# Kernel optimization log

Measured on AMD Instinct MI355X. Metric: run time of the kernel, lower is better.

## Reference

```python
import jax, jax.numpy as jnp
import numpy as np

B, S, H, NH = 2, 2048, 1024, 16
HD = H // NH
R = 4
LORA_SCALE = 16.0 / 4.0  # lora_alpha / r


def lora_linear(x, W, b, A, Bm):
    # x: [b,t,in]; W: [out,in]; A: [r,in]; Bm: [out,r]
    base = jnp.einsum('bti,oi->bto', x, W) + b
    lora = jnp.einsum('btr,or->bto', jnp.einsum('bti,ri->btr', x, A), Bm)
    return base + LORA_SCALE * lora


def setup_inputs() -> dict:
    key = jax.random.key(0)
    ks = jax.random.split(key, 14)
    std = 1.0 / np.sqrt(H)
    d = {
        'hidden_states': jax.random.normal(ks[0], (B, S, H), dtype=jnp.float32),
        'attention_mask': jnp.zeros((B, 1, 1, S), dtype=jnp.float32),
    }
    for i, nm in enumerate(['q', 'k', 'v']):
        d[f'W{nm}'] = jax.random.normal(ks[1 + 4 * i], (H, H), dtype=jnp.float32) * std
        d[f'b{nm}'] = jnp.zeros((H,), dtype=jnp.float32)
        d[f'A{nm}'] = jax.random.normal(ks[2 + 4 * i], (R, H), dtype=jnp.float32) * std
        d[f'B{nm}'] = jnp.zeros((H, R), dtype=jnp.float32) + 0.01 * jax.random.normal(ks[3 + 4 * i], (H, R), dtype=jnp.float32)
    return d


def reference(hidden_states, attention_mask, Wq, bq, Aq, Bq, Wk, bk, Ak, Bk, Wv, bv, Av, Bv):
    def heads(p):  # [b,t,(h d)] -> [b,h,t,d]
        return p.reshape(B, S, NH, HD).transpose(0, 2, 1, 3)

    q = heads(lora_linear(hidden_states, Wq, bq, Aq, Bq))
    k = heads(lora_linear(hidden_states, Wk, bk, Ak, Bk))
    v = heads(lora_linear(hidden_states, Wv, bv, Av, Bv))

    scores = jnp.einsum('bhqd,bhkd->bhqk', q, k) / jnp.sqrt(jnp.float32(HD))
    causal = jnp.tril(jnp.ones((S, S), dtype=scores.dtype))
    causal = (1.0 - causal) * -10000.0  # [S,S], broadcast over b,h
    scores = scores + attention_mask + causal[None, None]
    weights = jax.nn.softmax(scores, axis=-1)  # dropout p=0 -> identity (eval)
    ctx = jnp.einsum('bhqk,bhkd->bhqd', weights, v)
    return ctx.transpose(0, 2, 1, 3).reshape(B, S, H)
```

## Files before the change

kernel.cpp:

```cpp
#include <hip/hip_runtime.h>
#include <stdint.h>

#define B_ 2
#define S_ 2048
#define H_ 1024
#define NH_ 16
#define HD_ 64
#define M_ 4096
#define LOG2E 1.44269504089f

typedef unsigned short u16;
typedef __bf16 bf16x8 __attribute__((ext_vector_type(8)));
typedef float  f32x4  __attribute__((ext_vector_type(4)));

#if __has_builtin(__builtin_amdgcn_exp2f)
#define EXP2(x) __builtin_amdgcn_exp2f(x)
#else
#define EXP2(x) exp2f(x)
#endif

#define WAITV4() asm volatile("s_waitcnt vmcnt(4)" ::: "memory")
#define WAITV0() asm volatile("s_waitcnt vmcnt(0)" ::: "memory")
#define SCHED0() __builtin_amdgcn_sched_barrier(0)

__device__ inline u16 f2bf(float f) {
  union { float f; uint32_t u; } a; a.f = f;
  uint32_t r = a.u + 0x7FFFu + ((a.u >> 16) & 1u);
  return (u16)(r >> 16);
}

__device__ inline void gload_lds16(const void* g, void* l) {
  __builtin_amdgcn_global_load_lds((const __attribute__((address_space(1))) void*)g,
                                   (__attribute__((address_space(3))) void*)l, 16, 0, 0);
}

__global__ __launch_bounds__(256) void cvt_kernel(
    const float* __restrict__ x,
    const float* __restrict__ wq, const float* __restrict__ wk, const float* __restrict__ wv,
    const float* __restrict__ Aq, const float* __restrict__ Ak, const float* __restrict__ Av,
    const float* __restrict__ LBq, const float* __restrict__ LBk, const float* __restrict__ LBv,
    const float* __restrict__ amask,
    u16* __restrict__ xbf, u16* __restrict__ wbf, float* __restrict__ maskl2e) {
  const int XN = M_ * H_;
  const int WN = H_ * H_;
  const int total = XN + 3 * WN;
  int idx = (blockIdx.x * 256 + threadIdx.x) * 4;
  if (idx < XN) {
    float4 v = *(const float4*)(x + idx);
    *(ushort4*)(xbf + idx) = make_ushort4(f2bf(v.x), f2bf(v.y), f2bf(v.z), f2bf(v.w));
  } else if (idx < total) {
    int j = idx - XN; int p = j >> 20; int off = j & (WN - 1);
    const float* W  = (p == 0) ? wq : (p == 1 ? wk : wv);
    const float* A  = (p == 0) ? Aq : (p == 1 ? Ak : Av);
    const float* LB = (p == 0) ? LBq : (p == 1 ? LBk : LBv);
    int n = off >> 10, k = off & 1023;
    float4 v  = *(const float4*)(W + off);
    f32x4 lb  = *(const f32x4*)&LB[n * 4];
    float4 a0 = *(const float4*)(A + k);
    float4 a1 = *(const float4*)(A + 1024 + k);
    float4 a2 = *(const float4*)(A + 2048 + k);
    float4 a3 = *(const float4*)(A + 3072 + k);
    v.x += 4.f * (lb.x * a0.x + lb.y * a1.x + lb.z * a2.x + lb.w * a3.x);
    v.y += 4.f * (lb.x * a0.y + lb.y * a1.y + lb.z * a2.y + lb.w * a3.y);
    v.z += 4.f * (lb.x * a0.z + lb.y * a1.z + lb.z * a2.z + lb.w * a3.z);
    v.w += 4.f * (lb.x * a0.w + lb.y * a1.w + lb.z * a2.w + lb.w * a3.w);
    *(ushort4*)(wbf + (p << 20) + off) = make_ushort4(f2bf(v.x), f2bf(v.y), f2bf(v.z), f2bf(v.w));
  } else {
    int mi = idx - total;
    if (mi < B_ * S_) {
      float4 mv = *(const float4*)(amask + mi);
      mv.x *= LOG2E; mv.y *= LOG2E; mv.z *= LOG2E; mv.w *= LOG2E;
      *(float4*)(maskl2e + mi) = mv;
    }
  }
}

template<int P>
__device__ __forceinline__ void gemm_body(
    const u16* __restrict__ xbf, const u16* __restrict__ wbf,
    const float* __restrict__ bias, u16* __restrict__ qkv,
    u16* __restrict__ As, u16* __restrict__ Bs) {
  const int n0 = blockIdx.x * 128;
  const int m0 = blockIdx.y * 128;
  const u16* Wp = wbf + (P << 20);
  const int tid = threadIdx.x, lane = tid & 63, w = tid >> 6;
  const int g = lane >> 4, q15 = lane & 15;
  const int wr = w >> 1, wc = w & 1;
  const f32x4 fzero = {0.f, 0.f, 0.f, 0.f};
  f32x4 acc[4][4];
#pragma unroll
  for (int mi = 0; mi < 4; ++mi)
#pragma unroll
    for (int ni = 0; ni < 4; ++ni) acc[mi][ni] = fzero;
  const int srow = lane >> 2;

  auto STAGE = [&](int buf, int k0) {
#pragma unroll
    for (int j = 0; j < 2; ++j) {
      int c = w * 2 + j;
      int row = c * 16 + srow;
      int uu = (lane & 3) ^ ((row >> 1) & 3);
      gload_lds16(xbf + (size_t)(m0 + row) * 1024 + k0 + uu * 8, As + buf * 4096 + c * 512);
      gload_lds16(Wp  + (size_t)(n0 + row) * 1024 + k0 + uu * 8, Bs + buf * 4096 + c * 512);
    }
  };

  STAGE(0, 0);
  STAGE(1, 32);
  int c0 = 0, c1 = 1, c2 = 2;
#pragma unroll 1
  for (int t = 0; t < 32; ++t) {
    if (t < 31) WAITV4(); else WAITV0();
    SCHED0();
    __builtin_amdgcn_s_barrier();
    if (t + 2 < 32) STAGE(c2, (t + 2) * 32);
    const u16* Ab = As + c0 * 4096;
    const u16* Bb = Bs + c0 * 4096;
    bf16x8 af[4], bfr[4];
#pragma unroll
    for (int mi = 0; mi < 4; ++mi) {
      int r = wr * 64 + mi * 16 + q15;
      af[mi] = *(const bf16x8*)&Ab[r * 32 + ((g ^ ((r >> 1) & 3)) * 8)];
    }
#pragma unroll
    for (int ni = 0; ni < 4; ++ni) {
      int r = wc * 64 + ni * 16 + q15;
      bfr[ni] = *(const bf16x8*)&Bb[r * 32 + ((g ^ ((r >> 1) & 3)) * 8)];
    }
    __builtin_amdgcn_s_setprio(1);
#pragma unroll
    for (int mi = 0; mi < 4; ++mi)
#pragma unroll
      for (int ni = 0; ni < 4; ++ni) {
        if (P == 2)
          acc[mi][ni] = __builtin_amdgcn_mfma_f32_16x16x32_bf16(af[mi], bfr[ni], acc[mi][ni], 0, 0, 0);
        else
          acc[mi][ni] = __builtin_amdgcn_mfma_f32_16x16x32_bf16(bfr[ni], af[mi], acc[mi][ni], 0, 0, 0);
      }
    __builtin_amdgcn_s_setprio(0);
    int tmp = c0; c0 = c1; c1 = c2; c2 = tmp;
  }

  if (P != 2) {
#pragma unroll
    for (int ni = 0; ni < 4; ++ni) {
      int nb = n0 + wc * 64 + ni * 16 + g * 4;
      f32x4 bi = *(const f32x4*)&bias[nb];
      int h = nb >> 6, dbase = nb & 63;
#pragma unroll
      for (int mi = 0; mi < 4; ++mi) {
        int m = m0 + wr * 64 + mi * 16 + q15;
        int bb = m >> 11, s = m & 2047;
        size_t bhs = (size_t)(bb * 16 + h) * 2048 + s;
        float v0 = acc[mi][ni][0] + bi.x, v1 = acc[mi][ni][1] + bi.y;
        float v2 = acc[mi][ni][2] + bi.z, v3 = acc[mi][ni][3] + bi.w;
        size_t addr;
        if (P == 0) {
          const float qs = 0.125f * LOG2E;
          v0 *= qs; v1 *= qs; v2 *= qs; v3 *= qs;
          addr = bhs * 64 + dbase;
        } else {
          int pos = (((dbase >> 3) ^ (s & 7)) << 3) | (dbase & 7);
          addr = 4194304 + bhs * 64 + pos;
        }
        *(ushort4*)&qkv[addr] = make_ushort4(f2bf(v0), f2bf(v1), f2bf(v2), f2bf(v3));
      }
    }
  } else {
    float biasv[4];
#pragma unroll
    for (int ni = 0; ni < 4; ++ni) biasv[ni] = bias[n0 + wc * 64 + ni * 16 + q15];
#pragma unroll
    for (int mi = 0; mi < 4; ++mi) {
      int mbase = m0 + wr * 64 + mi * 16 + g * 4;
      int bb = mbase >> 11, sbase = mbase & 2047;
      int sr = sbase & 31;
      int cba = (((sr >> 4) & 1) << 2) | (((sr >> 2) & 3) << 3);
      int sp = (sbase & 32) | cba;
#pragma unroll
      for (int ni = 0; ni < 4; ++ni) {
        int n = n0 + wc * 64 + ni * 16 + q15;
        int d = n & 63, h = n >> 6;
        int spp = (((sp >> 3) ^ (d & 7)) << 3) | (sp & 7);
        size_t addr = 8388608 + ((size_t)(bb * 16 + h) * 64 + d) * 2048 + (sbase & ~63) + spp;
        *(ushort4*)&qkv[addr] = make_ushort4(
            f2bf(acc[mi][ni][0] + biasv[ni]), f2bf(acc[mi][ni][1] + biasv[ni]),
            f2bf(acc[mi][ni][2] + biasv[ni]), f2bf(acc[mi][ni][3] + biasv[ni]));
      }
    }
  }
}

__global__ __launch_bounds__(256) void qkv_gemm(
    const u16* __restrict__ xbf, const u16* __restrict__ wbf,
    const float* __restrict__ bq, const float* __restrict__ bk, const float* __restrict__ bv,
    u16* __restrict__ qkv) {
  __shared__ __align__(16) u16 As[3 * 4096];
  __shared__ __align__(16) u16 Bs[3 * 4096];
  switch (blockIdx.z) {
    case 0: gemm_body<0>(xbf, wbf, bq, qkv, As, Bs); break;
    case 1: gemm_body<1>(xbf, wbf, bk, qkv, As, Bs); break;
    default: gemm_body<2>(xbf, wbf, bv, qkv, As, Bs); break;
  }
}

__global__ __launch_bounds__(256, 2) void attn_kernel(
    const u16* __restrict__ qkv, const float* __restrict__ maskl2e, float* __restrict__ out) {
  const int bid = blockIdx.x;
  const int bh = (bid & 7) * 4 + ((bid >> 3) & 3);
  const int qt = 15 - (bid >> 5);
  const int b = bh >> 4, h = bh & 15;
  const int tid = threadIdx.x, lane = tid & 63, w = tid >> 6;
  const int g = lane >> 4, ql = lane & 15;
  const u16* Qb = qkv + (size_t)bh * 131072;
  const u16* Kb = qkv + 4194304 + (size_t)bh * 131072;
  const u16* Vb = qkv + 8388608 + (size_t)bh * 131072;
  const float* Mb = maskl2e + b * 2048;
  __shared__ __align__(16) u16 Ks[2][64][64];
  __shared__ __align__(16) u16 Vs[2][64][64];

  auto STAGE = [&](int nb, int kb) {
#pragma unroll
    for (int j = 0; j < 2; ++j) {
      int rl = w * 16 + j * 8 + (lane >> 3);
      gload_lds16(Kb + (size_t)(kb + rl) * 64 + (lane & 7) * 8, &Ks[nb][w * 16 + j * 8][0]);
      gload_lds16(Vb + (size_t)rl * 2048 + kb + (lane & 7) * 8, &Vs[nb][w * 16 + j * 8][0]);
    }
  };

  const int qbase = qt * 128 + w * 32;
  bf16x8 qf[2][2];
#pragma unroll
  for (int qg = 0; qg < 2; ++qg)
#pragma unroll
    for (int ks = 0; ks < 2; ++ks)
      qf[qg][ks] = *(const bf16x8*)&Qb[(size_t)(qbase + qg * 16 + ql) * 64 + ks * 32 + g * 8];
  const f32x4 fzero = {0.f, 0.f, 0.f, 0.f};
  f32x4 acc[2][4];
#pragma unroll
  for (int qg = 0; qg < 2; ++qg)
#pragma unroll
    for (int dt = 0; dt < 4; ++dt) acc[qg][dt] = fzero;
  float mrun[2] = {-1e30f, -1e30f}, lrun[2] = {0.f, 0.f};
  const int nt = 2 * qt + 2;

  f32x4 mkC[4], mkN[4];
  STAGE(0, 0);
#pragma unroll
  for (int k16 = 0; k16 < 4; ++k16) mkC[k16] = *(const f32x4*)&Mb[k16 * 16 + g * 4];

#pragma unroll 1
  for (int t = 0; t < nt; ++t) {
    WAITV0();
    SCHED0();
    __builtin_amdgcn_s_barrier();
    const int kb = t * 64;
    if (t + 1 < nt) {
      STAGE((t + 1) & 1, kb + 64);
#pragma unroll
      for (int k16 = 0; k16 < 4; ++k16) mkN[k16] = *(const f32x4*)&Mb[kb + 64 + k16 * 16 + g * 4];
    }
    const int cb = t & 1;
    f32x4 st[2][4];
    __builtin_amdgcn_s_setprio(1);
#pragma unroll
    for (int k16 = 0; k16 < 4; ++k16) {
      bf16x8 kf0 = *(const bf16x8*)&Ks[cb][k16 * 16 + ql][(g ^ (ql & 7)) * 8];
      bf16x8 kf1 = *(const bf16x8*)&Ks[cb][k16 * 16 + ql][((4 + g) ^ (ql & 7)) * 8];
      st[0][k16] = __builtin_amdgcn_mfma_f32_16x16x32_bf16(kf0, qf[0][0], mkC[k16], 0, 0, 0);
      st[0][k16] = __builtin_amdgcn_mfma_f32_16x16x32_bf16(kf1, qf[0][1], st[0][k16], 0, 0, 0);
      st[1][k16] = __builtin_amdgcn_mfma_f32_16x16x32_bf16(kf0, qf[1][0], mkC[k16], 0, 0, 0);
      st[1][k16] = __builtin_amdgcn_mfma_f32_16x16x32_bf16(kf1, qf[1][1], st[1][k16], 0, 0, 0);
    }
    __builtin_amdgcn_s_setprio(0);
    bf16x8 pfv[2][2];
#pragma unroll
    for (int qg = 0; qg < 2; ++qg) {
      const int qq = qbase + qg * 16 + ql;
      const bool needm = (kb + 63 > qbase + qg * 16);
      float sc[16];
#pragma unroll
      for (int k16 = 0; k16 < 4; ++k16)
#pragma unroll
        for (int r = 0; r < 4; ++r) {
          float sv = st[qg][k16][r];
          if (needm) { int key = kb + k16 * 16 + g * 4 + r; sv = (key > qq) ? -1e30f : sv; }
          sc[k16 * 4 + r] = sv;
        }
      float m8[8], m4[4];
#pragma unroll
      for (int i = 0; i < 8; ++i) m8[i] = fmaxf(sc[i], sc[i + 8]);
#pragma unroll
      for (int i = 0; i < 4; ++i) m4[i] = fmaxf(m8[i], m8[i + 4]);
      float pmax = fmaxf(fmaxf(m4[0], m4[1]), fmaxf(m4[2], m4[3]));
      if (!__all(pmax <= mrun[qg] + 8.f)) {
        float pm = fmaxf(pmax, __shfl_xor(pmax, 16, 64));
        pm = fmaxf(pm, __shfl_xor(pm, 32, 64));
        const float mt = fmaxf(mrun[qg], pm);
        const float scale = EXP2(mrun[qg] - mt);
        lrun[qg] *= scale;
#pragma unroll
        for (int dt = 0; dt < 4; ++dt) acc[qg][dt] *= scale;
        mrun[qg] = mt;
      }
      float pv[16];
#pragma unroll
      for (int i = 0; i < 16; ++i) pv[i] = EXP2(sc[i] - mrun[qg]);
      float s8[8], s4[4];
#pragma unroll
      for (int i = 0; i < 8; ++i) s8[i] = pv[i] + pv[i + 8];
#pragma unroll
      for (int i = 0; i < 4; ++i) s4[i] = s8[i] + s8[i + 4];
      lrun[qg] += (s4[0] + s4[1]) + (s4[2] + s4[3]);
#pragma unroll
      for (int ksub = 0; ksub < 2; ++ksub)
#pragma unroll
        for (int j = 0; j < 4; ++j) {
          pfv[qg][ksub][j]     = (__bf16)pv[ksub * 8 + j];
          pfv[qg][ksub][4 + j] = (__bf16)pv[ksub * 8 + 4 + j];
        }
    }
    __builtin_amdgcn_s_setprio(1);
#pragma unroll
    for (int dt = 0; dt < 4; ++dt)
#pragma unroll
      for (int ksub = 0; ksub < 2; ++ksub) {
        bf16x8 vf = *(const bf16x8*)&Vs[cb][dt * 16 + ql][((ksub * 4 + g) ^ (ql & 7)) * 8];
        acc[0][dt] = __builtin_amdgcn_mfma_f32_16x16x32_bf16(vf, pfv[0][ksub], acc[0][dt], 0, 0, 0);
        acc[1][dt] = __builtin_amdgcn_mfma_f32_16x16x32_bf16(vf, pfv[1][ksub], acc[1][dt], 0, 0, 0);
      }
    __builtin_amdgcn_s_setprio(0);
#pragma unroll
    for (int k16 = 0; k16 < 4; ++k16) mkC[k16] = mkN[k16];
  }

#pragma unroll
  for (int qg = 0; qg < 2; ++qg) {
    float lsum = lrun[qg];
    lsum += __shfl_xor(lsum, 16, 64);
    lsum += __shfl_xor(lsum, 32, 64);
    const float inv = 1.f / lsum;
    const int qq = qbase + qg * 16 + ql;
#pragma unroll
    for (int dt = 0; dt < 4; ++dt) {
      f32x4 o = acc[qg][dt] * inv;
      *(f32x4*)&out[((size_t)b * 2048 + qq) * 1024 + h * 64 + dt * 16 + g * 4] = o;
    }
  }
}

extern "C" void kernel_launch(void* const* d_in, const int* in_sizes, int n_in,
                              void* d_out, int out_size, void* d_ws, size_t ws_size,
                              hipStream_t stream) {
  const float* x  = (const float*)d_in[0];
  const float* am = (const float*)d_in[1];
  const float* Wq = (const float*)d_in[2];
  const float* bq = (const float*)d_in[3];
  const float* Aq = (const float*)d_in[4];
  const float* Bq = (const float*)d_in[5];
  const float* Wk = (const float*)d_in[6];
  const float* bk = (const float*)d_in[7];
  const float* Ak = (const float*)d_in[8];
  const float* Bk = (const float*)d_in[9];
  const float* Wv = (const float*)d_in[10];
  const float* bv = (const float*)d_in[11];
  const float* Av = (const float*)d_in[12];
  const float* Bv = (const float*)d_in[13];
  float* out = (float*)d_out;

  u16* xbf   = (u16*)d_ws;
  u16* wbf   = xbf + 4194304;
  u16* qkv   = wbf + 3145728;
  float* mk  = (float*)(qkv + 12582912);

  cvt_kernel<<<7172, 256, 0, stream>>>(x, Wq, Wk, Wv, Aq, Ak, Av, Bq, Bk, Bv, am, xbf, wbf, mk);
  qkv_gemm<<<dim3(8, 32, 3), 256, 0, stream>>>(xbf, wbf, bq, bk, bv, qkv);
  attn_kernel<<<512, 256, 0, stream>>>(qkv, mk, out);
}
```

Before: 106.1 us.

## Split causal attention into balanced per-wave key chunks with a merge pass

Each wave now handles a pair of 32-row query groups (p and 63-p) and a fixed slice of 11 key tiles, which balances the causal work across waves. Partial accumulators are stored as bf16 in reused workspace and the m/l statistics in a side buffer, and a new merge kernel combines them with log-sum-exp weights. K/V are loaded straight from global memory into registers instead of being staged through LDS with barriers, and occupancy rises to three blocks per CU. The cost is an extra kernel launch, extra global traffic for the partials, and lower precision in the bf16 partial accumulators.

```diff
diff --git a/kernel.cpp b/kernel.cpp
--- a/kernel.cpp
+++ b/kernel.cpp
@@ -27,6 +27,9 @@
   union { float f; uint32_t u; } a; a.f = f;
   uint32_t r = a.u + 0x7FFFu + ((a.u >> 16) & 1u);
   return (u16)(r >> 16);
+}
+__device__ inline float bf2f(u16 v) {
+  union { uint32_t u; float f; } a; a.u = ((uint32_t)v) << 16; return a.f;
 }
 
 __device__ inline void gload_lds16(const void* g, void* l) {
@@ -204,148 +207,218 @@
   }
 }
 
-__global__ __launch_bounds__(256, 2) void attn_kernel(
-    const u16* __restrict__ qkv, const float* __restrict__ maskl2e, float* __restrict__ out) {
+__global__ __launch_bounds__(256, 3) void attn_kernel(
+    const u16* __restrict__ qkv, const float* __restrict__ maskl2e, float* __restrict__ out,
+    u16* __restrict__ pacc, float* __restrict__ pml) {
   const int bid = blockIdx.x;
-  const int bh = (bid & 7) * 4 + ((bid >> 3) & 3);
-  const int qt = 15 - (bid >> 5);
+  const int w = threadIdx.x >> 6, lane = threadIdx.x & 63;
+  const int lg = lane >> 4, ql = lane & 15, m7 = ql & 7;
+  const int xcd = bid & 7, jj = bid >> 3;
+  const int wi = jj * 4 + w;
+  const int bhl = wi / 96, r96 = wi - bhl * 96;
+  const int bh = xcd * 4 + bhl;
+  const int p = r96 / 3, s = r96 - (r96 / 3) * 3;
+  const int lo = s * 11, hi = lo + 11;
+  const int nA = (p >> 1) + 1;
   const int b = bh >> 4, h = bh & 15;
-  const int tid = threadIdx.x, lane = tid & 63, w = tid >> 6;
-  const int g = lane >> 4, ql = lane & 15;
   const u16* Qb = qkv + (size_t)bh * 131072;
   const u16* Kb = qkv + 4194304 + (size_t)bh * 131072;
   const u16* Vb = qkv + 8388608 + (size_t)bh * 131072;
   const float* Mb = maskl2e + b * 2048;
-  __shared__ __align__(16) u16 Ks[2][64][64];
-  __shared__ __align__(16) u16 Vs[2][64][64];
-
-  auto STAGE = [&](int nb, int kb) {
-#pragma unroll
-    for (int j = 0; j < 2; ++j) {
-      int rl = w * 16 + j * 8 + (lane >> 3);
-      gload_lds16(Kb + (size_t)(kb + rl) * 64 + (lane & 7) * 8, &Ks[nb][w * 16 + j * 8][0]);
-      gload_lds16(Vb + (size_t)rl * 2048 + kb + (lane & 7) * 8, &Vs[nb][w * 16 + j * 8][0]);
-    }
-  };
-
-  const int qbase = qt * 128 + w * 32;
-  bf16x8 qf[2][2];
-#pragma unroll
-  for (int qg = 0; qg < 2; ++qg)
-#pragma unroll
-    for (int ks = 0; ks < 2; ++ks)
-      qf[qg][ks] = *(const bf16x8*)&Qb[(size_t)(qbase + qg * 16 + ql) * 64 + ks * 32 + g * 8];
+  const int u0 = lg ^ m7, u1 = (4 + lg) ^ m7;
   const f32x4 fzero = {0.f, 0.f, 0.f, 0.f};
-  f32x4 acc[2][4];
-#pragma unroll
-  for (int qg = 0; qg < 2; ++qg)
-#pragma unroll
-    for (int dt = 0; dt < 4; ++dt) acc[qg][dt] = fzero;
-  float mrun[2] = {-1e30f, -1e30f}, lrun[2] = {0.f, 0.f};
-  const int nt = 2 * qt + 2;
-
-  f32x4 mkC[4], mkN[4];
-  STAGE(0, 0);
-#pragma unroll
-  for (int k16 = 0; k16 < 4; ++k16) mkC[k16] = *(const f32x4*)&Mb[k16 * 16 + g * 4];
+
+  bf16x8 kA[8]; f32x4 mA[4]; bf16x8 vA[8];
+
+#define LOADK(KT) do { const int kb_ = (KT) * 64; \
+  _Pragma("unroll") for (int k16 = 0; k16 < 4; ++k16) { \
+    kA[k16*2]   = *(const bf16x8*)&Kb[(size_t)(kb_ + k16*16 + ql) * 64 + u0 * 8]; \
+    kA[k16*2+1] = *(const bf16x8*)&Kb[(size_t)(kb_ + k16*16 + ql) * 64 + u1 * 8]; \
+    mA[k16]     = *(const f32x4*)&Mb[kb_ + k16*16 + lg*4]; } } while (0)
+#define LOADV(KT) do { const int kb_ = (KT) * 64; \
+  _Pragma("unroll") for (int dt = 0; dt < 4; ++dt) { \
+    vA[dt*2]   = *(const bf16x8*)&Vb[(size_t)(dt*16 + ql) * 2048 + kb_ + u0 * 8]; \
+    vA[dt*2+1] = *(const bf16x8*)&Vb[(size_t)(dt*16 + ql) * 2048 + kb_ + u1 * 8]; } } while (0)
 
 #pragma unroll 1
-  for (int t = 0; t < nt; ++t) {
-    WAITV0();
-    SCHED0();
-    __builtin_amdgcn_s_barrier();
-    const int kb = t * 64;
-    if (t + 1 < nt) {
-      STAGE((t + 1) & 1, kb + 64);
-#pragma unroll
-      for (int k16 = 0; k16 < 4; ++k16) mkN[k16] = *(const f32x4*)&Mb[kb + 64 + k16 * 16 + g * 4];
-    }
-    const int cb = t & 1;
-    f32x4 st[2][4];
-    __builtin_amdgcn_s_setprio(1);
-#pragma unroll
-    for (int k16 = 0; k16 < 4; ++k16) {
-      bf16x8 kf0 = *(const bf16x8*)&Ks[cb][k16 * 16 + ql][(g ^ (ql & 7)) * 8];
-      bf16x8 kf1 = *(const bf16x8*)&Ks[cb][k16 * 16 + ql][((4 + g) ^ (ql & 7)) * 8];
-      st[0][k16] = __builtin_amdgcn_mfma_f32_16x16x32_bf16(kf0, qf[0][0], mkC[k16], 0, 0, 0);
-      st[0][k16] = __builtin_amdgcn_mfma_f32_16x16x32_bf16(kf1, qf[0][1], st[0][k16], 0, 0, 0);
-      st[1][k16] = __builtin_amdgcn_mfma_f32_16x16x32_bf16(kf0, qf[1][0], mkC[k16], 0, 0, 0);
-      st[1][k16] = __builtin_amdgcn_mfma_f32_16x16x32_bf16(kf1, qf[1][1], st[1][k16], 0, 0, 0);
-    }
-    __builtin_amdgcn_s_setprio(0);
-    bf16x8 pfv[2][2];
+  for (int ph = 0; ph < 2; ++ph) {
+    const int G   = ph ? (63 - p) : p;
+    const int kt0 = ph ? ((lo - nA > 0) ? lo - nA : 0) : ((lo < nA) ? lo : nA);
+    const int kt1 = ph ? (hi - nA) : ((hi < nA) ? hi : nA);
+    if (kt0 >= kt1) continue;
+    const int lastT = G >> 1;
+    bf16x8 qf[2][2];
+#pragma unroll
+    for (int qg = 0; qg < 2; ++qg)
+#pragma unroll
+      for (int ks = 0; ks < 2; ++ks)
+        qf[qg][ks] = *(const bf16x8*)&Qb[(size_t)(G*32 + qg*16 + ql) * 64 + ks*32 + lg*8];
+    f32x4 acc[2][4];
+#pragma unroll
+    for (int qg = 0; qg < 2; ++qg)
+#pragma unroll
+      for (int dt = 0; dt < 4; ++dt) acc[qg][dt] = fzero;
+    float mrun[2] = {-1e30f, -1e30f}, lrun[2] = {0.f, 0.f};
+
+    LOADK(kt0);
+#pragma unroll 1
+    for (int kt = kt0; kt < kt1; ++kt) {
+      LOADV(kt);
+      const int kb = kt * 64;
+      f32x4 st[2][4];
+      __builtin_amdgcn_s_setprio(1);
+#pragma unroll
+      for (int k16 = 0; k16 < 4; ++k16) {
+        st[0][k16] = __builtin_amdgcn_mfma_f32_16x16x32_bf16(kA[k16*2],   qf[0][0], mA[k16], 0, 0, 0);
+        st[0][k16] = __builtin_amdgcn_mfma_f32_16x16x32_bf16(kA[k16*2+1], qf[0][1], st[0][k16], 0, 0, 0);
+        st[1][k16] = __builtin_amdgcn_mfma_f32_16x16x32_bf16(kA[k16*2],   qf[1][0], mA[k16], 0, 0, 0);
+        st[1][k16] = __builtin_amdgcn_mfma_f32_16x16x32_bf16(kA[k16*2+1], qf[1][1], st[1][k16], 0, 0, 0);
+      }
+      __builtin_amdgcn_s_setprio(0);
+      if (kt + 1 < kt1) LOADK(kt + 1);
+      const bool needm = (kt == lastT);
+      bf16x8 pfv0[2], pfv1[2];
+#pragma unroll
+      for (int qg = 0; qg < 2; ++qg) {
+        const int q = G*32 + qg*16 + ql;
+        float sc[16];
+#pragma unroll
+        for (int k16 = 0; k16 < 4; ++k16)
+#pragma unroll
+          for (int rr = 0; rr < 4; ++rr) {
+            float sv = st[qg][k16][rr];
+            if (needm) { int key = kb + k16*16 + lg*4 + rr; sv = (key > q) ? -1e30f : sv; }
+            sc[k16*4 + rr] = sv;
+          }
+        float m8[8], m4[4];
+#pragma unroll
+        for (int i = 0; i < 8; ++i) m8[i] = fmaxf(sc[i], sc[i + 8]);
+#pragma unroll
+        for (int i = 0; i < 4; ++i) m4[i] = fmaxf(m8[i], m8[i + 4]);
+        float pmax = fmaxf(fmaxf(m4[0], m4[1]), fmaxf(m4[2], m4[3]));
+        if (!__all(pmax <= mrun[qg] + 8.f)) {
+          float pm = fmaxf(pmax, __shfl_xor(pmax, 16, 64));
+          pm = fmaxf(pm, __shfl_xor(pm, 32, 64));
+          const float mt = fmaxf(mrun[qg], pm);
+          const float scale = EXP2(mrun[qg] - mt);
+          lrun[qg] *= scale;
+#pragma unroll
+          for (int dt = 0; dt < 4; ++dt) acc[qg][dt] *= scale;
+          mrun[qg] = mt;
+        }
+        float pv[16];
+#pragma unroll
+        for (int i = 0; i < 16; ++i) pv[i] = EXP2(sc[i] - mrun[qg]);
+        float s8[8], s4[4];
+#pragma unroll
+        for (int i = 0; i < 8; ++i) s8[i] = pv[i] + pv[i + 8];
+#pragma unroll
+        for (int i = 0; i < 4; ++i) s4[i] = s8[i] + s8[i + 4];
+        lrun[qg] += (s4[0] + s4[1]) + (s4[2] + s4[3]);
+        bf16x8* pf = qg ? pfv1 : pfv0;
+#pragma unroll
+        for (int ksub = 0; ksub < 2; ++ksub)
+#pragma unroll
+          for (int j2 = 0; j2 < 4; ++j2) {
+            pf[ksub][j2]     = (__bf16)pv[ksub*8 + j2];
+            pf[ksub][4 + j2] = (__bf16)pv[ksub*8 + 4 + j2];
+          }
+      }
+      __builtin_amdgcn_s_setprio(1);
+#pragma unroll
+      for (int dt = 0; dt < 4; ++dt)
+#pragma unroll
+        for (int ksub = 0; ksub < 2; ++ksub) {
+          acc[0][dt] = __builtin_amdgcn_mfma_f32_16x16x32_bf16(vA[dt*2+ksub], pfv0[ksub], acc[0][dt], 0, 0, 0);
+          acc[1][dt] = __builtin_amdgcn_mfma_f32_16x16x32_bf16(vA[dt*2+ksub], pfv1[ksub], acc[1][dt], 0, 0, 0);
+        }
+      __builtin_amdgcn_s_setprio(0);
+    }
+
+    float lsum[2];
 #pragma unroll
     for (int qg = 0; qg < 2; ++qg) {
-      const int qq = qbase + qg * 16 + ql;
-      const bool needm = (kb + 63 > qbase + qg * 16);
-      float sc[16];
-#pragma unroll
-      for (int k16 = 0; k16 < 4; ++k16)
-#pragma unroll
-        for (int r = 0; r < 4; ++r) {
-          float sv = st[qg][k16][r];
-          if (needm) { int key = kb + k16 * 16 + g * 4 + r; sv = (key > qq) ? -1e30f : sv; }
-          sc[k16 * 4 + r] = sv;
-        }
-      float m8[8], m4[4];
-#pragma unroll
-      for (int i = 0; i < 8; ++i) m8[i] = fmaxf(sc[i], sc[i + 8]);
-#pragma unroll
-      for (int i = 0; i < 4; ++i) m4[i] = fmaxf(m8[i], m8[i + 4]);
-      float pmax = fmaxf(fmaxf(m4[0], m4[1]), fmaxf(m4[2], m4[3]));
-      if (!__all(pmax <= mrun[qg] + 8.f)) {
-        float pm = fmaxf(pmax, __shfl_xor(pmax, 16, 64));
-        pm = fmaxf(pm, __shfl_xor(pm, 32, 64));
-        const float mt = fmaxf(mrun[qg], pm);
-        const float scale = EXP2(mrun[qg] - mt);
-        lrun[qg] *= scale;
-#pragma unroll
-        for (int dt = 0; dt < 4; ++dt) acc[qg][dt] *= scale;
-        mrun[qg] = mt;
-      }
-      float pv[16];
-#pragma unroll
-      for (int i = 0; i < 16; ++i) pv[i] = EXP2(sc[i] - mrun[qg]);
-      float s8[8], s4[4];
-#pragma unroll
-      for (int i = 0; i < 8; ++i) s8[i] = pv[i] + pv[i + 8];
-#pragma unroll
-      for (int i = 0; i < 4; ++i) s4[i] = s8[i] + s8[i + 4];
-      lrun[qg] += (s4[0] + s4[1]) + (s4[2] + s4[3]);
-#pragma unroll
-      for (int ksub = 0; ksub < 2; ++ksub)
-#pragma unroll
-        for (int j = 0; j < 4; ++j) {
-          pfv[qg][ksub][j]     = (__bf16)pv[ksub * 8 + j];
-          pfv[qg][ksub][4 + j] = (__bf16)pv[ksub * 8 + 4 + j];
-        }
-    }
-    __builtin_amdgcn_s_setprio(1);
-#pragma unroll
-    for (int dt = 0; dt < 4; ++dt)
-#pragma unroll
-      for (int ksub = 0; ksub < 2; ++ksub) {
-        bf16x8 vf = *(const bf16x8*)&Vs[cb][dt * 16 + ql][((ksub * 4 + g) ^ (ql & 7)) * 8];
-        acc[0][dt] = __builtin_amdgcn_mfma_f32_16x16x32_bf16(vf, pfv[0][ksub], acc[0][dt], 0, 0, 0);
-        acc[1][dt] = __builtin_amdgcn_mfma_f32_16x16x32_bf16(vf, pfv[1][ksub], acc[1][dt], 0, 0, 0);
-      }
-    __builtin_amdgcn_s_setprio(0);
-#pragma unroll
-    for (int k16 = 0; k16 < 4; ++k16) mkC[k16] = mkN[k16];
-  }
-
-#pragma unroll
-  for (int qg = 0; qg < 2; ++qg) {
-    float lsum = lrun[qg];
-    lsum += __shfl_xor(lsum, 16, 64);
-    lsum += __shfl_xor(lsum, 32, 64);
-    const float inv = 1.f / lsum;
-    const int qq = qbase + qg * 16 + ql;
-#pragma unroll
-    for (int dt = 0; dt < 4; ++dt) {
-      f32x4 o = acc[qg][dt] * inv;
-      *(f32x4*)&out[((size_t)b * 2048 + qq) * 1024 + h * 64 + dt * 16 + g * 4] = o;
-    }
+      float ls = lrun[qg];
+      ls += __shfl_xor(ls, 16, 64);
+      ls += __shfl_xor(ls, 32, 64);
+      lsum[qg] = ls;
+    }
+    const bool writer = ph ? (s == 2) : (s == 0);
+    if (writer) {
+#pragma unroll
+      for (int qg = 0; qg < 2; ++qg)
+#pragma unroll
+        for (int dt = 0; dt < 4; ++dt)
+          *(f32x4*)&out[((size_t)b * 2048 + G*32 + qg*16 + ql) * 1024 + h*64 + dt*16 + lg*4] = acc[qg][dt];
+    } else {
+      int rec;
+      if (ph == 0) rec = bh * 10 + (G - 22);
+      else rec = (s == 1) ? (320 + bh * 32 + (G - 32))
+                          : (1344 + bh * 20 + (G - 44));
+      u16* pr = pacc + (size_t)rec * 2048;
+#pragma unroll
+      for (int qg = 0; qg < 2; ++qg)
+#pragma unroll
+        for (int dt = 0; dt < 4; ++dt)
+          *(ushort4*)&pr[(qg*16 + ql) * 64 + dt*16 + lg*4] =
+              make_ushort4(f2bf(acc[qg][dt][0]), f2bf(acc[qg][dt][1]),
+                           f2bf(acc[qg][dt][2]), f2bf(acc[qg][dt][3]));
+    }
+    if (lg == 0) {
+      float* pb = pml + (size_t)((bh * 64 + G) * 3 + s) * 64;
+#pragma unroll
+      for (int qg = 0; qg < 2; ++qg) {
+        pb[(qg*16 + ql) * 2]     = mrun[qg];
+        pb[(qg*16 + ql) * 2 + 1] = lsum[qg];
+      }
+    }
+  }
+#undef LOADK
+#undef LOADV
+}
+
+__global__ __launch_bounds__(128) void merge_kernel(
+    const u16* __restrict__ pacc, const float* __restrict__ pml, float* __restrict__ out) {
+  const int mu = blockIdx.x;
+  const int bh = mu >> 6, g = mu & 63;
+  const int b = bh >> 4, h = bh & 15;
+  const int t = threadIdx.x;
+  const int row = t >> 2, dc = (t & 3) * 16;
+  const int pb = (bh * 64 + g) * 3;
+  const int wslot = (g < 32) ? 0 : 2;
+  bool has1 = false, has2 = false;
+  const u16 *bp1 = nullptr, *bp2 = nullptr;
+  if (g < 32) {
+    if (g >= 22) { has1 = true; bp1 = pacc + (size_t)(bh * 10 + (g - 22)) * 2048; }
+  } else {
+    has1 = true; bp1 = pacc + (size_t)(320 + bh * 32 + (g - 32)) * 2048;
+    if (g >= 44) { has2 = true; bp2 = pacc + (size_t)(1344 + bh * 20 + (g - 44)) * 2048; }
+  }
+  const float mw = pml[(size_t)(pb + wslot) * 64 + row * 2];
+  const float lw = pml[(size_t)(pb + wslot) * 64 + row * 2 + 1];
+  float m1 = -1e30f, l1 = 0.f, m2 = -1e30f, l2 = 0.f;
+  if (has1) { m1 = pml[(size_t)(pb + 1) * 64 + row * 2]; l1 = pml[(size_t)(pb + 1) * 64 + row * 2 + 1]; }
+  if (has2) { m2 = pml[(size_t)(pb + 0) * 64 + row * 2]; l2 = pml[(size_t)(pb + 0) * 64 + row * 2 + 1]; }
+  const float M = fmaxf(mw, fmaxf(m1, m2));
+  const float ww = EXP2(mw - M);
+  const float w1 = has1 ? EXP2(m1 - M) : 0.f;
+  const float w2 = has2 ? EXP2(m2 - M) : 0.f;
+  const float inv = 1.f / (ww * lw + w1 * l1 + w2 * l2);
+  float* op = out + ((size_t)b * 2048 + g * 32 + row) * 1024 + h * 64 + dc;
+#pragma unroll
+  for (int j2 = 0; j2 < 4; ++j2) {
+    f32x4 o = *(const f32x4*)(op + j2 * 4);
+    o *= ww;
+    if (has1) {
+      ushort4 u = *(const ushort4*)(bp1 + row * 64 + dc + j2 * 4);
+      o[0] += w1 * bf2f(u.x); o[1] += w1 * bf2f(u.y); o[2] += w1 * bf2f(u.z); o[3] += w1 * bf2f(u.w);
+    }
+    if (has2) {
+      ushort4 u = *(const ushort4*)(bp2 + row * 64 + dc + j2 * 4);
+      o[0] += w2 * bf2f(u.x); o[1] += w2 * bf2f(u.y); o[2] += w2 * bf2f(u.z); o[3] += w2 * bf2f(u.w);
+    }
+    o *= inv;
+    *(f32x4*)(op + j2 * 4) = o;
   }
 }
 
@@ -372,8 +445,11 @@
   u16* wbf   = xbf + 4194304;
   u16* qkv   = wbf + 3145728;
   float* mk  = (float*)(qkv + 12582912);
+  u16* pacc  = xbf;
+  float* pml = (float*)wbf;
 
   cvt_kernel<<<7172, 256, 0, stream>>>(x, Wq, Wk, Wv, Aq, Ak, Av, Bq, Bk, Bv, am, xbf, wbf, mk);
   qkv_gemm<<<dim3(8, 32, 3), 256, 0, stream>>>(xbf, wbf, bq, bk, bv, qkv);
-  attn_kernel<<<512, 256, 0, stream>>>(qkv, mk, out);
-}
+  attn_kernel<<<768, 256, 0, stream>>>(qkv, mk, out, pacc, pml);
+  merge_kernel<<<2048, 128, 0, stream>>>(pacc, pml, out);
+}
```

Result: slower. 185.4 us (+74.7%).
